# Kernel optimization log

Measured on AMD Instinct MI355X. Metric: run time of the kernel, lower is better.

The kernel has to match this reference:

```python
import jax, jax.numpy as jnp
import numpy as np

R = 2            # interleaving factor (init kwarg r)
C = 16           # feature channels
N = 500_000      # number of sparse voxels
GRID = 256       # fine-grid extent per axis


def setup_inputs() -> dict:
    key = jax.random.key(0)
    kc, kf = jax.random.split(key)
    coords = jax.random.randint(kc, (N, 3), 0, GRID, dtype=jnp.int32)
    feats = jax.random.normal(kf, (N, C), dtype=jnp.float32)
    return {"feats": feats, "coords": coords}


def reference(feats, coords):
    # Sparse interleaving: group fine voxels into coarse voxels of size R^3,
    # scattering each point's C features into the slot given by its intra-cell offset.
    r2 = R * R
    r3 = r2 * R
    n = coords.shape[0]
    base = coords // R                      # [N,3] coarse voxel coords
    off = coords % R                        # [N,3] intra-cell offset
    offset_idx = off[:, 0] * r2 + off[:, 1] * R + off[:, 2]  # [N]

    # jit-compatible unique: fixed output size (worst case: all points distinct)
    unique_coords, inv = jnp.unique(base, axis=0, size=n, fill_value=-1,
                                    return_inverse=True)
    inv = inv.reshape(-1)                   # [N] row in aggregated output

    # target column = offset_idx*C + channel  (matches torch scatter_ layout)
    col = offset_idx[:, None] * C + jnp.arange(C, dtype=offset_idx.dtype)[None, :]  # [N,C]
    agg = jnp.zeros((n, C * r3), dtype=feats.dtype)
    agg = agg.at[inv[:, None], col].set(feats)
    return unique_coords.astype(jnp.int32), agg
```

## Files before the change

kernel.cpp:

```cpp
#include <hip/hip_runtime.h>


#define WORDS 65536u
#define SENTINEL 0xFFFFFFFFu

typedef float v4f __attribute__((ext_vector_type(4)));

__global__ void mark_kernel(const int* __restrict__ coords,
                            unsigned* __restrict__ bitmap,
                            unsigned* __restrict__ winner, int n) {
    int i = blockIdx.x * 256 + threadIdx.x;
    if (i >= n) return;
    int cx = coords[3 * i], cy = coords[3 * i + 1], cz = coords[3 * i + 2];
    unsigned key = ((unsigned)(cx >> 1) << 14) | ((unsigned)(cy >> 1) << 7) |
                   (unsigned)(cz >> 1);
    unsigned off = ((unsigned)(cx & 1) << 2) | ((unsigned)(cy & 1) << 1) |
                   (unsigned)(cz & 1);
    atomicOr(&bitmap[key >> 5], 1u << (key & 31));
    atomicMax(&winner[key * 8u + off], (unsigned)i + 1u);
}

__global__ void scanall_kernel(const unsigned* __restrict__ bitmap,
                               unsigned* __restrict__ chunkExcl,
                               unsigned* __restrict__ U) {
    __shared__ unsigned sh[256];
    int t = threadIdx.x;
    const uint4* b4 = (const uint4*)bitmap;
    unsigned base = (unsigned)t * 64u;
    unsigned s = 0;
#pragma unroll 8
    for (unsigned j = 0; j < 64u; ++j) {
        uint4 v = b4[base + j];
        s += __popc(v.x) + __popc(v.y) + __popc(v.z) + __popc(v.w);
    }
    unsigned x = s;
    sh[t] = x; __syncthreads();
    for (int d = 1; d < 256; d <<= 1) {
        unsigned y = (t >= d) ? sh[t - d] : 0u;
        __syncthreads();
        x += y; sh[t] = x; __syncthreads();
    }
    chunkExcl[t] = x - s;
    if (t == 255) *U = x;
}

__global__ __launch_bounds__(256)
void rank_kernel(const unsigned* __restrict__ bitmap,
                 const unsigned* __restrict__ chunkExcl,
                 const unsigned* __restrict__ Uptr,
                 unsigned* __restrict__ cells,
                 float* __restrict__ coords_out, int n) {
    __shared__ unsigned sh[256];
    int t = threadIdx.x;
    unsigned w = blockIdx.x * 256 + t;
    unsigned word = bitmap[w];
    unsigned cnt = __popc(word);
    unsigned x = cnt;
    sh[t] = x; __syncthreads();
    for (int d = 1; d < 256; d <<= 1) {
        unsigned y = (t >= d) ? sh[t - d] : 0u;
        __syncthreads();
        x += y; sh[t] = x; __syncthreads();
    }
    unsigned rb = chunkExcl[blockIdx.x] + x - cnt;
    while (word) {
        int k = __ffs(word) - 1;
        word &= word - 1;
        unsigned cell = w * 32u + (unsigned)k;
        cells[rb] = cell;
        coords_out[3 * rb + 0] = (float)(cell >> 14);
        coords_out[3 * rb + 1] = (float)((cell >> 7) & 127u);
        coords_out[3 * rb + 2] = (float)(cell & 127u);
        ++rb;
    }
    unsigned Uv = *Uptr;
    unsigned gid = blockIdx.x * 256u + (unsigned)t;
    unsigned nth = gridDim.x * 256u;
    for (unsigned r = Uv + gid; r < (unsigned)n; r += nth) {
        cells[r] = SENTINEL;
        coords_out[3 * r + 0] = -1.0f;
        coords_out[3 * r + 1] = -1.0f;
        coords_out[3 * r + 2] = -1.0f;
    }
}

__global__ void gather_kernel(const float* __restrict__ feats,
                              const unsigned* __restrict__ winner,
                              const unsigned* __restrict__ cells,
                              float* __restrict__ agg, int total4) {
    int j = blockIdx.x * 256 + threadIdx.x;
    if (j >= total4) return;
    unsigned row = (unsigned)j >> 5;
    unsigned cell = cells[row];
    v4f v = (v4f)(0.f);
    if (cell != SENTINEL) {
        unsigned off = ((unsigned)j >> 2) & 7u;
        unsigned w = winner[cell * 8u + off];
        if (w) {
            unsigned c4 = (unsigned)j & 3u;
            v = ((const v4f*)feats)[(size_t)(w - 1u) * 4u + c4];
        }
    }
    __builtin_nontemporal_store(v, (v4f*)agg + j);
}

extern "C" void kernel_launch(void* const* d_in, const int* in_sizes, int n_in,
                              void* d_out, int out_size, void* d_ws, size_t ws_size,
                              hipStream_t stream) {
    const float* feats = (const float*)d_in[0];
    const int* coords  = (const int*)d_in[1];
    int n = in_sizes[1] / 3;

    float* out        = (float*)d_out;
    float* coords_out = out;
    float* agg        = out + (size_t)3 * n;

    unsigned* bitmap    = (unsigned*)d_ws;
    unsigned* winner    = bitmap + WORDS;
    unsigned* chunkExcl = winner + (size_t)WORDS * 256u;
    unsigned* U         = chunkExcl + 256;
    unsigned* cells     = U + 4;

    (void)hipMemsetAsync(d_ws, 0, (size_t)(WORDS + (size_t)WORDS * 256u) * 4u,
                         stream);

    int nb = (n + 255) / 256;
    mark_kernel<<<nb, 256, 0, stream>>>(coords, bitmap, winner, n);
    scanall_kernel<<<1, 256, 0, stream>>>(bitmap, chunkExcl, U);
    rank_kernel<<<WORDS / 256, 256, 0, stream>>>(bitmap, chunkExcl, U, cells,
                                                 coords_out, n);
    int total4 = n * 32;
    gather_kernel<<<(total4 + 255) / 256, 256, 0, stream>>>(feats, winner, cells,
                                                            agg, total4);
}
```

Baseline: 391.1 us.

## Index winner table by compacted rank and fuse scan into rank kernel

Replaces the dense per-cell winner table with a compact table indexed by each coarse cell's rank, computed in a new winner kernel from stored packed keys and per-word rank bases. This shrinks the workspace memset and lets the gather read winners sequentially instead of through a cells indirection. The single-block scan is folded into the rank kernel, with every block redundantly rescanning the whole bitmap. In exchange it adds an extra pass over the points and extra bitmap reads.

```diff
diff --git a/kernel.cpp b/kernel.cpp
--- a/kernel.cpp
+++ b/kernel.cpp
@@ -2,13 +2,12 @@
 
 
 #define WORDS 65536u
-#define SENTINEL 0xFFFFFFFFu
 
 typedef float v4f __attribute__((ext_vector_type(4)));
 
 __global__ void mark_kernel(const int* __restrict__ coords,
                             unsigned* __restrict__ bitmap,
-                            unsigned* __restrict__ winner, int n) {
+                            unsigned* __restrict__ keys, int n) {
     int i = blockIdx.x * 256 + threadIdx.x;
     if (i >= n) return;
     int cx = coords[3 * i], cy = coords[3 * i + 1], cz = coords[3 * i + 2];
@@ -16,15 +15,19 @@
                    (unsigned)(cz >> 1);
     unsigned off = ((unsigned)(cx & 1) << 2) | ((unsigned)(cy & 1) << 1) |
                    (unsigned)(cz & 1);
+    keys[i] = (key << 3) | off;
     atomicOr(&bitmap[key >> 5], 1u << (key & 31));
-    atomicMax(&winner[key * 8u + off], (unsigned)i + 1u);
 }
 
-__global__ void scanall_kernel(const unsigned* __restrict__ bitmap,
-                               unsigned* __restrict__ chunkExcl,
-                               unsigned* __restrict__ U) {
+__global__ __launch_bounds__(256)
+void rankscan_kernel(const unsigned* __restrict__ bitmap,
+                     unsigned* __restrict__ rank_base,
+                     float* __restrict__ coords_out, int n) {
     __shared__ unsigned sh[256];
+    __shared__ unsigned shChunkExcl, shU;
     int t = threadIdx.x;
+    int b = blockIdx.x;
+
     const uint4* b4 = (const uint4*)bitmap;
     unsigned base = (unsigned)t * 64u;
     unsigned s = 0;
@@ -40,67 +43,66 @@
         __syncthreads();
         x += y; sh[t] = x; __syncthreads();
     }
-    chunkExcl[t] = x - s;
-    if (t == 255) *U = x;
-}
+    if (t == b) shChunkExcl = x - s;
+    if (t == 255) shU = x;
+    __syncthreads();
+    unsigned chunkExcl = shChunkExcl;
+    unsigned U = shU;
+    __syncthreads();
 
-__global__ __launch_bounds__(256)
-void rank_kernel(const unsigned* __restrict__ bitmap,
-                 const unsigned* __restrict__ chunkExcl,
-                 const unsigned* __restrict__ Uptr,
-                 unsigned* __restrict__ cells,
-                 float* __restrict__ coords_out, int n) {
-    __shared__ unsigned sh[256];
-    int t = threadIdx.x;
-    unsigned w = blockIdx.x * 256 + t;
+    unsigned w = (unsigned)b * 256u + (unsigned)t;
     unsigned word = bitmap[w];
     unsigned cnt = __popc(word);
-    unsigned x = cnt;
+    x = cnt;
     sh[t] = x; __syncthreads();
     for (int d = 1; d < 256; d <<= 1) {
         unsigned y = (t >= d) ? sh[t - d] : 0u;
         __syncthreads();
         x += y; sh[t] = x; __syncthreads();
     }
-    unsigned rb = chunkExcl[blockIdx.x] + x - cnt;
+    unsigned rb = chunkExcl + x - cnt;
+    rank_base[w] = rb;
     while (word) {
         int k = __ffs(word) - 1;
         word &= word - 1;
         unsigned cell = w * 32u + (unsigned)k;
-        cells[rb] = cell;
         coords_out[3 * rb + 0] = (float)(cell >> 14);
         coords_out[3 * rb + 1] = (float)((cell >> 7) & 127u);
         coords_out[3 * rb + 2] = (float)(cell & 127u);
         ++rb;
     }
-    unsigned Uv = *Uptr;
-    unsigned gid = blockIdx.x * 256u + (unsigned)t;
+    unsigned gid = (unsigned)b * 256u + (unsigned)t;
     unsigned nth = gridDim.x * 256u;
-    for (unsigned r = Uv + gid; r < (unsigned)n; r += nth) {
-        cells[r] = SENTINEL;
+    for (unsigned r = U + gid; r < (unsigned)n; r += nth) {
         coords_out[3 * r + 0] = -1.0f;
         coords_out[3 * r + 1] = -1.0f;
         coords_out[3 * r + 2] = -1.0f;
     }
 }
 
+__global__ void winner_kernel(const unsigned* __restrict__ keys,
+                              const unsigned* __restrict__ bitmap,
+                              const unsigned* __restrict__ rank_base,
+                              unsigned* __restrict__ winner, int n) {
+    int i = blockIdx.x * 256 + threadIdx.x;
+    if (i >= n) return;
+    unsigned pk = keys[i];
+    unsigned key = pk >> 3, off = pk & 7u;
+    unsigned wd = key >> 5;
+    unsigned r = rank_base[wd] + __popc(bitmap[wd] & ((1u << (key & 31)) - 1u));
+    atomicMax(&winner[r * 8u + off], (unsigned)i + 1u);
+}
+
 __global__ void gather_kernel(const float* __restrict__ feats,
                               const unsigned* __restrict__ winner,
-                              const unsigned* __restrict__ cells,
                               float* __restrict__ agg, int total4) {
     int j = blockIdx.x * 256 + threadIdx.x;
     if (j >= total4) return;
-    unsigned row = (unsigned)j >> 5;
-    unsigned cell = cells[row];
+    int slot = j >> 2;
+    int c4 = j & 3;
+    unsigned w = __builtin_nontemporal_load(&winner[slot]);
     v4f v = (v4f)(0.f);
-    if (cell != SENTINEL) {
-        unsigned off = ((unsigned)j >> 2) & 7u;
-        unsigned w = winner[cell * 8u + off];
-        if (w) {
-            unsigned c4 = (unsigned)j & 3u;
-            v = ((const v4f*)feats)[(size_t)(w - 1u) * 4u + c4];
-        }
-    }
+    if (w) v = ((const v4f*)feats)[(size_t)(w - 1u) * 4u + c4];
     __builtin_nontemporal_store(v, (v4f*)agg + j);
 }
 
@@ -117,19 +119,18 @@
 
     unsigned* bitmap    = (unsigned*)d_ws;
     unsigned* winner    = bitmap + WORDS;
-    unsigned* chunkExcl = winner + (size_t)WORDS * 256u;
-    unsigned* U         = chunkExcl + 256;
-    unsigned* cells     = U + 4;
+    unsigned* rank_base = winner + (size_t)8 * n;
+    unsigned* keys      = rank_base + WORDS;
 
-    (void)hipMemsetAsync(d_ws, 0, (size_t)(WORDS + (size_t)WORDS * 256u) * 4u,
+    (void)hipMemsetAsync(d_ws, 0, (WORDS + (size_t)8 * n) * sizeof(unsigned),
                          stream);
 
     int nb = (n + 255) / 256;
-    mark_kernel<<<nb, 256, 0, stream>>>(coords, bitmap, winner, n);
-    scanall_kernel<<<1, 256, 0, stream>>>(bitmap, chunkExcl, U);
-    rank_kernel<<<WORDS / 256, 256, 0, stream>>>(bitmap, chunkExcl, U, cells,
-                                                 coords_out, n);
+    mark_kernel<<<nb, 256, 0, stream>>>(coords, bitmap, keys, n);
+    rankscan_kernel<<<WORDS / 256, 256, 0, stream>>>(bitmap, rank_base,
+                                                     coords_out, n);
+    winner_kernel<<<nb, 256, 0, stream>>>(keys, bitmap, rank_base, winner, n);
     int total4 = n * 32;
-    gather_kernel<<<(total4 + 255) / 256, 256, 0, stream>>>(feats, winner, cells,
-                                                            agg, total4);
+    gather_kernel<<<(total4 + 255) / 256, 256, 0, stream>>>(feats, winner, agg,
+                                                            total4);
 }
```

Result: faster. 361.4 us (-7.6%).
